# Kernel optimization log

Hardware: AMD Instinct MI355X
Metric: run time of the kernel (lower is better)

## Reference

```python
import jax, jax.numpy as jnp
import numpy as np

TK = 3          # number of temporal scales (wavedec level = TK-1)
SK = 3          # spatial rank count per scale (SK-1 rank-1 terms + residual)
INPUT_LEN = 256
N_NODES = 256
K = 32          # randomized-SVD sketch size
INV_SQRT2 = np.float32(1.0 / np.sqrt(2.0))


def haar_wavedec(x, levels):
    # x: (..., L) with L divisible by 2**levels; pywt haar, mode='zero', even L
    # returns [cD1, cD2, ..., cD_levels, cA_levels]  (== pywt.wavedec(...)[::-1])
    coeffs = []
    for _ in range(levels):
        L = x.shape[-1]
        pairs = x.reshape(x.shape[:-1] + (L // 2, 2))
        a, b = pairs[..., 0], pairs[..., 1]
        coeffs.append((a - b) * INV_SQRT2)  # detail cD
        x = (a + b) * INV_SQRT2             # approx cA
    coeffs.append(x)
    return coeffs


def setup_inputs() -> dict:
    key = jax.random.key(0)
    kx, kp = jax.random.split(key)
    x = jax.random.normal(kx, (4, INPUT_LEN, 64, N_NODES), dtype=jnp.float32)
    p = jax.random.normal(kp, (N_NODES, K), dtype=jnp.float32)
    return {"x": x, "p": p}


def reference(x, p):
    # x: (B, T, c, n) -> permute(0,2,3,1) -> (B, c, n, T)
    xw = jnp.transpose(x, (0, 2, 3, 1))
    coeffs = haar_wavedec(xw, TK - 1)  # TK tensors (B, c, n, L_i)
    res = []
    for xi in coeffs:
        if SK == 1:
            res.append(xi)
            continue
        xt = jnp.transpose(xi, (0, 3, 1, 2))          # (B, L, c, n)
        z = xt @ p                                     # (B, L, c, k)
        q, _ = jnp.linalg.qr(z)                        # reduced: (B, L, c, k)
        y = jnp.einsum('blck,blcn->blkn', q, xt)       # (B, L, k, n)
        u, s, vh = jnp.linalg.svd(y, full_matrices=False)  # u:(B,L,k,k) s:(B,L,k) vh:(B,L,k,n)
        u = q @ u                                      # (B, L, c, k)
        # rank-1 terms s_j * u_j v_j^T for j < SK-1, vectorized over j
        terms = jnp.einsum('blcj,blj,bljn->jblcn',
                           u[..., :SK - 1], s[..., :SK - 1], vh[..., :SK - 1, :])
        terms = jnp.transpose(terms, (0, 1, 3, 4, 2))  # (SK-1, B, c, n, L)
        resid = xi - terms.sum(axis=0)
        for j in range(SK - 1):
            res.append(terms[j])
        res.append(resid)
    # left-pad last dim to INPUT_LEN, then stack -> (TK*SK, B, c, n, INPUT_LEN)
    res = [jnp.pad(r, ((0, 0), (0, 0), (0, 0), (INPUT_LEN - r.shape[-1], 0))) for r in res]
    return jnp.stack(res)
```

## Files before the change

kernel.cpp:

```cpp
#include <hip/hip_runtime.h>

#define IS2f 0.70710678118654752440f

#define WS_Z   0ul
#define WS_G   2097152ul
#define WS_H   3145728ul
#define WS_SU  4194304ul
#define WS_VV  4325376ul
#define WS_B   4849664ul

#define WSYNC() asm volatile("" ::: "memory")

__device__ __forceinline__ float frcp(float v){ return __builtin_amdgcn_rcpf(v); }
__device__ __forceinline__ float frsq(float v){ return __builtin_amdgcn_rsqf(v); }
__device__ __forceinline__ float fsq (float v){ return __builtin_amdgcn_sqrtf(v); }
__device__ __forceinline__ float readlane_f(float v, int sl){
  return __uint_as_float(__builtin_amdgcn_readlane(__float_as_uint(v), sl));
}

__device__ __forceinline__ void decode_pid(int pid, int& ci, int& b, int& l, int& L){
  if (pid < 512)      { ci = 0; b = pid >> 7; l = pid & 127; L = 128; }
  else if (pid < 768) { int q = pid - 512; ci = 1; b = q >> 6; l = q & 63; L = 64; }
  else                { int q = pid - 768; ci = 2; b = q >> 6; l = q & 63; L = 64; }
}
__device__ __forceinline__ int su_base(int ci){ return ci==0 ? 0 : (ci==1 ? 65536 : 98304); }
__device__ __forceinline__ int vv_base(int ci){ return ci==0 ? 0 : (ci==1 ? 262144 : 393216); }
__device__ __forceinline__ int tpp(int r, int m){ return (m==0) ? r  : (r+m)%31; }
__device__ __forceinline__ int tqq(int r, int m){ return (m==0) ? 31 : (r+31-m)%31; }
__device__ __forceinline__ void jparam(float app, float aqq, float apq,
                                       float& cc, float& ss){
  float tau = (aqq - app) * frcp(2.f*apq);
  float tt  = ((tau>=0.f)?1.f:-1.f) * frcp(fabsf(tau) + fsq(fmaf(tau,tau,1.f)));
  float c   = frsq(fmaf(tt,tt,1.f));
  float s   = tt*c;
  bool ok = fabsf(apq) > 1e-28f;
  cc = ok ? c : 1.f;
  ss = ok ? s : 0.f;
}

#define PTS 260

__global__ __launch_bounds__(512) void k_fact(const float* __restrict__ x,
                                              const float* __restrict__ p,
                                              float* __restrict__ ws, int storeB){
  __shared__ __align__(16) float Ms[64*256];
  __shared__ __align__(16) float Zs[64*32];
  __shared__ __align__(16) float Pt[32*PTS];
  __shared__ __align__(16) float Bn[32*PTS];
  __shared__ float Gl[33*33];

  int pid = blockIdx.x, tid = threadIdx.x;
  int ci,b,l,L; decode_pid(pid,ci,b,l,L);

  {
    const float4* p4 = (const float4*)p;
    #pragma unroll
    for (int e=0;e<4;++e){
      int idx = tid + 512*e;
      int n = idx >> 3, k4 = idx & 7;
      float4 v = p4[idx];
      Pt[(4*k4+0)*PTS + n] = v.x;
      Pt[(4*k4+1)*PTS + n] = v.y;
      Pt[(4*k4+2)*PTS + n] = v.z;
      Pt[(4*k4+3)*PTS + n] = v.w;
    }
  }
  const float4* x4 = (const float4*)x;
  float4* Ms4 = (float4*)Ms;
  if (ci == 0){
    size_t base = ((size_t)(b*256 + 2*l) * 64) * 64;
    #pragma unroll
    for (int e=0;e<8;++e){
      int f = tid + 512*e;
      float4 A = x4[base + f];
      float4 Bv = x4[base + 4096 + f];
      float4 m;
      m.x=(A.x-Bv.x)*IS2f; m.y=(A.y-Bv.y)*IS2f; m.z=(A.z-Bv.z)*IS2f; m.w=(A.w-Bv.w)*IS2f;
      Ms4[f] = m;
    }
  } else {
    float sg = (ci==1) ? -0.5f : 0.5f;
    size_t base = ((size_t)(b*256 + 4*l) * 64) * 64;
    #pragma unroll
    for (int e=0;e<8;++e){
      int f = tid + 512*e;
      float4 A = x4[base + f];
      float4 B1 = x4[base + 4096 + f];
      float4 C1 = x4[base + 8192 + f];
      float4 D1 = x4[base + 12288 + f];
      float4 m;
      m.x=(A.x+B1.x)*0.5f + (C1.x+D1.x)*sg;
      m.y=(A.y+B1.y)*0.5f + (C1.y+D1.y)*sg;
      m.z=(A.z+B1.z)*0.5f + (C1.z+D1.z)*sg;
      m.w=(A.w+B1.w)*0.5f + (C1.w+D1.w)*sg;
      Ms4[f] = m;
    }
  }
  __syncthreads();

  {
    int k = tid & 31, c0 = tid >> 5;
    float acc[4] = {0,0,0,0};
    for (int n4=0;n4<64;++n4){
      float4 pv = *(const float4*)&Pt[k*PTS + 4*n4];
      #pragma unroll
      for (int i=0;i<4;++i){
        float4 m = Ms4[(c0*4+i)*64 + n4];
        acc[i] += m.x*pv.x + m.y*pv.y + m.z*pv.z + m.w*pv.w;
      }
    }
    #pragma unroll
    for (int i=0;i<4;++i){
      int c = c0*4 + i;
      Zs[c*32+k] = acc[i];
      ws[WS_Z + (size_t)pid*2048 + c*32 + k] = acc[i];
    }
  }
  __syncthreads();

  {
    int kk = tid & 31, j0 = tid >> 5;
    float ga[2] = {0,0};
    for (int c=0;c<64;++c){
      float zk = Zs[c*32+kk];
      #pragma unroll
      for (int e=0;e<2;++e) ga[e] += Zs[c*32 + j0 + 16*e] * zk;
    }
    #pragma unroll
    for (int e=0;e<2;++e)
      Gl[(j0+16*e)*33 + kk] = ga[e];
  }

  {
    int n4 = tid & 63, kg = tid >> 6;
    float4 facc[4];
    #pragma unroll
    for (int kq=0;kq<4;++kq){ facc[kq].x=0.f; facc[kq].y=0.f; facc[kq].z=0.f; facc[kq].w=0.f; }
    for (int c=0;c<64;++c){
      float4 mv = Ms4[c*64 + n4];
      float4 z1 = *(const float4*)&Zs[c*32 + kg*4];
      float zz[4] = {z1.x,z1.y,z1.z,z1.w};
      #pragma unroll
      for (int kq=0;kq<4;++kq){
        facc[kq].x += zz[kq]*mv.x; facc[kq].y += zz[kq]*mv.y;
        facc[kq].z += zz[kq]*mv.z; facc[kq].w += zz[kq]*mv.w;
      }
    }
    #pragma unroll
    for (int kq=0;kq<4;++kq){
      int krow = kg*4 + kq;
      *(float4*)&Bn[krow*PTS + 4*n4] = facc[kq];
      if (storeB)
        *(float4*)&ws[WS_B + (size_t)pid*8192 + (size_t)krow*256 + 4*n4] = facc[kq];
    }
  }
  __syncthreads();

  {
    int jlane = tid & 31, grp = tid >> 5;
    for (int k=0;k<32;++k){
      float gkk  = Gl[k*33+k];
      float ginv = frcp(gkk);
      float gkj  = Gl[k*33+jlane];
      float av[2], bv[2];
      #pragma unroll
      for (int e=0;e<2;++e){
        int i = k+1+grp+16*e; int ii = (i<32)? i : 31;
        av[e] = Gl[ii*33+jlane];
        bv[e] = Gl[k*33+ii];
      }
      WSYNC();
      #pragma unroll
      for (int e=0;e<2;++e){
        int i = k+1+grp+16*e;
        if (i < 32) Gl[i*33+jlane] = av[e] - bv[e]*gkj*ginv;
      }
      __syncthreads();
    }
    float sv[2];
    #pragma unroll
    for (int e=0;e<2;++e){
      int i = grp+16*e;
      sv[e] = Gl[i*33+jlane] * frsq(Gl[i*33+i]);
    }
    WSYNC();
    #pragma unroll
    for (int e=0;e<2;++e){
      int i = grp+16*e;
      Gl[i*33+jlane] = sv[e];
    }
  }
  __syncthreads();

  #pragma unroll
  for (int e=0;e<2;++e){
    int idx = tid + 512*e;
    ws[WS_G + (size_t)pid*1024 + idx] = Gl[(idx>>5)*33 + (idx&31)];
  }

  if (tid < 256){
    int n = tid;
    float c[32];
    #pragma unroll
    for (int i=0;i<32;++i){
      float cv = Bn[i*PTS + n];
      #pragma unroll
      for (int k=0;k<i;++k) cv -= Gl[k*33+i]*c[k];
      c[i] = cv * frcp(Gl[i*33+i]);
    }
    #pragma unroll
    for (int i=0;i<32;++i) Bn[i*PTS + n] = c[i];
  }
  __syncthreads();

  {
    int kk = tid & 31, j0 = tid >> 5;
    float h[2] = {0,0};
    for (int n4=0;n4<64;++n4){
      float4 bk = *(const float4*)&Bn[kk*PTS + 4*n4];
      #pragma unroll
      for (int e=0;e<2;++e){
        float4 bj = *(const float4*)&Bn[(j0+16*e)*PTS + 4*n4];
        h[e] += bj.x*bk.x + bj.y*bk.y + bj.z*bk.z + bj.w*bk.w;
      }
    }
    #pragma unroll
    for (int e=0;e<2;++e)
      ws[WS_H + (size_t)pid*1024 + (j0+16*e)*32 + kk] = h[e];
  }
}

#define NSWEEP 5

__global__ __launch_bounds__(128) void k_solve(const float* __restrict__ x,
                                               float* __restrict__ ws, int useB){
  __shared__ float Gs[32*33];
  __shared__ float Hb[2][32*33];
  __shared__ __align__(16) float Vb[2][32*36];
  __shared__ float cA2[2][16], sA2[2][16];
  __shared__ float ggs[2][32];
  __shared__ float uss[2][64];

  int pid = blockIdx.x, tid = threadIdx.x;
  int wave = tid >> 6;
  int lane = tid & 63;
  int jlane = tid & 31;
  int hlf  = (tid >> 5) & 1;
  int ci,b,l,L; decode_pid(pid,ci,b,l,L);

  #pragma unroll
  for (int e=0;e<8;++e){
    int idx = tid + 128*e; int i = idx>>5, j = idx&31;
    Gs[i*33+j]    = ws[WS_G + (size_t)pid*1024 + idx];
    Hb[0][i*33+j] = ws[WS_H + (size_t)pid*1024 + idx];
  }
  #pragma unroll
  for (int e=0;e<9;++e) Vb[0][tid + 128*e] = 0.f;
  __syncthreads();
  if (tid < 32) Vb[0][tid*36 + tid] = 1.f;
  __syncthreads();

  float dmx = (lane < 32) ? fabsf(Hb[0][jlane*33+jlane]) : 0.f;
  #pragma unroll
  for (int off=1; off<64; off<<=1) dmx = fmaxf(dmx, __shfl_xor(dmx, off));
  float thr = dmx * 3e-6f;

  int m2 = (lane >> 3) + 8*wave;
  int g  = lane & 7;
  int cur = 0;

  for (int sw=0; sw<NSWEEP; ++sw){
    for (int r=0; r<31; ++r){
      float* Hc = Hb[cur];
      float* Hn = Hb[cur^1];
      float4* Vc4 = (float4*)Vb[cur];
      float4* Vn4 = (float4*)Vb[cur^1];

      int m = lane & 15;
      int pm = tpp(r,m), qm = tqq(r,m);
      float apq = Hc[pm*33+qm];
      if (!__ballot(fabsf(apq) > thr)) continue;
      float app = Hc[pm*33+pm];
      float aqq = Hc[qm*33+qm];
      float cc, ssv; jparam(app, aqq, apq, cc, ssv);
      if (lane < 16){ cA2[wave][lane] = cc; sA2[wave][lane] = ssv; }
      WSYNC();

      int p2 = tpp(r,m2), q2 = tqq(r,m2);
      float c2 = cA2[wave][m2], s2 = sA2[wave][m2];

      float a_[2], b_[2], c_[2], d_[2], c1v[2], s1v[2];
      int p1v[2], q1v[2];
      #pragma unroll
      for (int e=0;e<2;++e){
        int m1 = g + 8*e;
        int p1 = tpp(r,m1), q1 = tqq(r,m1);
        p1v[e]=p1; q1v[e]=q1;
        c1v[e]=cA2[wave][m1]; s1v[e]=sA2[wave][m1];
        a_[e] = Hc[p1*33+p2]; b_[e] = Hc[p1*33+q2];
        c_[e] = Hc[q1*33+p2]; d_[e] = Hc[q1*33+q2];
      }
      float4 vp = Vc4[p2*9 + g];
      float4 vq = Vc4[q2*9 + g];

      #pragma unroll
      for (int e=0;e<2;++e){
        float c1 = c1v[e], s1 = s1v[e];
        float a1 = c1*a_[e] - s1*c_[e];
        float b1 = c1*b_[e] - s1*d_[e];
        float c1r= s1*a_[e] + c1*c_[e];
        float d1 = s1*b_[e] + c1*d_[e];
        Hn[p1v[e]*33+p2] = c2*a1 - s2*b1;
        Hn[p1v[e]*33+q2] = s2*a1 + c2*b1;
        Hn[q1v[e]*33+p2] = c2*c1r - s2*d1;
        Hn[q1v[e]*33+q2] = s2*c1r + c2*d1;
      }
      float4 np, nq;
      np.x = c2*vp.x - s2*vq.x;  nq.x = s2*vp.x + c2*vq.x;
      np.y = c2*vp.y - s2*vq.y;  nq.y = s2*vp.y + c2*vq.y;
      np.z = c2*vp.z - s2*vq.z;  nq.z = s2*vp.z + c2*vq.z;
      np.w = c2*vp.w - s2*vq.w;  nq.w = s2*vp.w + c2*vq.w;
      Vn4[p2*9 + g] = np;
      Vn4[q2*9 + g] = nq;
      __syncthreads();
      cur ^= 1;
    }
  }
  __syncthreads();
  if (wave == 1) return;

  float* Hs = Hb[cur];
  float* Vt = Vb[cur];

  float rdgr = frcp(Gs[jlane*33+jlane]);

  float dv = (lane < 32) ? Hs[jlane*33+jlane] : -3e38f;
  float m1r = dv;
  #pragma unroll
  for (int off=1; off<64; off<<=1) m1r = fmaxf(m1r, __shfl_xor(m1r, off));
  unsigned long long bm = __ballot(dv == m1r);
  int i0 = __ffsll((unsigned long long)bm) - 1;
  float dv2 = (lane == i0) ? -3e38f : dv;
  float m2r = dv2;
  #pragma unroll
  for (int off=1; off<64; off<<=1) m2r = fmaxf(m2r, __shfl_xor(m2r, off));
  unsigned long long bm2 = __ballot(dv2 == m2r);
  int i1 = __ffsll((unsigned long long)bm2) - 1;

  float lam = hlf ? m2r : m1r;
  int   ti  = hlf ? i1 : i0;
  float sj  = fsq(fmaxf(lam, 0.f)); sj = fmaxf(sj, 1e-12f);
  float s0 = readlane_f(sj, 0);
  float s1 = readlane_f(sj, 32);

  {
    float rr = Vt[ti*36 + jlane];
    float Greg[32];
    #pragma unroll
    for (int i=0;i<32;++i) Greg[i] = Gs[jlane*33+i];
    #pragma unroll
    for (int i=31;i>=0;--i){
      float ri = __shfl(rr,  hlf*32 + i);
      float di = __shfl(rdgr, i);
      float g  = ri * di;
      if (jlane == i) ggs[hlf][i] = g;
      if (jlane < i)  rr -= Greg[i]*g;
    }
  }
  WSYNC();

  {
    const float4* Z4 = (const float4*)(ws + WS_Z + (size_t)pid*2048);
    float u0 = 0.f, u1 = 0.f;
    #pragma unroll
    for (int k4=0;k4<8;++k4){
      float4 z = Z4[lane*8 + k4];
      u0 += z.x*ggs[0][k4*4+0] + z.y*ggs[0][k4*4+1] + z.z*ggs[0][k4*4+2] + z.w*ggs[0][k4*4+3];
      u1 += z.x*ggs[1][k4*4+0] + z.y*ggs[1][k4*4+1] + z.z*ggs[1][k4*4+2] + z.w*ggs[1][k4*4+3];
    }
    uss[0][lane] = u0; uss[1][lane] = u1;
    ws[WS_SU + su_base(ci) + ((size_t)(b*2+0)*64 + lane)*L + l] = s0*u0;
    ws[WS_SU + su_base(ci) + ((size_t)(b*2+1)*64 + lane)*L + l] = s1*u1;
  }
  WSYNC();

  float i0s = frcp(s0), i1s = frcp(s1);
  size_t vb0 = WS_VV + vv_base(ci) + ((size_t)(b*2+0)*L + l)*256 + lane*4;
  size_t vb1 = WS_VV + vv_base(ci) + ((size_t)(b*2+1)*L + l)*256 + lane*4;

  if (useB){
    const float4* B4 = (const float4*)(ws + WS_B + (size_t)pid*8192);
    float a0x=0,a0y=0,a0z=0,a0w=0, a1x=0,a1y=0,a1z=0,a1w=0;
    #pragma unroll 8
    for (int k=0;k<32;++k){
      float4 bv = B4[(size_t)k*64 + lane];
      float g0 = ggs[0][k], g1 = ggs[1][k];
      a0x += g0*bv.x; a0y += g0*bv.y; a0z += g0*bv.z; a0w += g0*bv.w;
      a1x += g1*bv.x; a1y += g1*bv.y; a1z += g1*bv.z; a1w += g1*bv.w;
    }
    float4 r0; r0.x=a0x*i0s; r0.y=a0y*i0s; r0.z=a0z*i0s; r0.w=a0w*i0s;
    float4 r1; r1.x=a1x*i1s; r1.y=a1y*i1s; r1.z=a1z*i1s; r1.w=a1w*i1s;
    *(float4*)(ws + vb0) = r0;
    *(float4*)(ws + vb1) = r1;
  } else {
    float a0x=0,a0y=0,a0z=0,a0w=0, a1x=0,a1y=0,a1z=0,a1w=0;
    const float4* x4 = (const float4*)x;
    if (ci == 0){
      size_t base = ((size_t)(b*256 + 2*l) * 64) * 64;
      #pragma unroll 2
      for (int c=0;c<64;++c){
        float4 A  = x4[base + c*64 + lane];
        float4 Bv = x4[base + 4096 + c*64 + lane];
        float mx=(A.x-Bv.x)*IS2f, my=(A.y-Bv.y)*IS2f, mz=(A.z-Bv.z)*IS2f, mw=(A.w-Bv.w)*IS2f;
        float uc0 = uss[0][c], uc1 = uss[1][c];
        a0x += uc0*mx; a0y += uc0*my; a0z += uc0*mz; a0w += uc0*mw;
        a1x += uc1*mx; a1y += uc1*my; a1z += uc1*mz; a1w += uc1*mw;
      }
    } else {
      float sg = (ci==1) ? -0.5f : 0.5f;
      size_t base = ((size_t)(b*256 + 4*l) * 64) * 64;
      #pragma unroll 2
      for (int c=0;c<64;++c){
        float4 A  = x4[base + c*64 + lane];
        float4 B1 = x4[base + 4096 + c*64 + lane];
        float4 C1 = x4[base + 8192 + c*64 + lane];
        float4 D1 = x4[base + 12288 + c*64 + lane];
        float mx=(A.x+B1.x)*0.5f + (C1.x+D1.x)*sg;
        float my=(A.y+B1.y)*0.5f + (C1.y+D1.y)*sg;
        float mz=(A.z+B1.z)*0.5f + (C1.z+D1.z)*sg;
        float mw=(A.w+B1.w)*0.5f + (C1.w+D1.w)*sg;
        float uc0 = uss[0][c], uc1 = uss[1][c];
        a0x += uc0*mx; a0y += uc0*my; a0z += uc0*mz; a0w += uc0*mw;
        a1x += uc1*mx; a1y += uc1*my; a1z += uc1*mz; a1w += uc1*mw;
      }
    }
    ws[vb0+0]=a0x*i0s; ws[vb0+1]=a0y*i0s; ws[vb0+2]=a0z*i0s; ws[vb0+3]=a0w*i0s;
    ws[vb1+0]=a1x*i1s; ws[vb1+1]=a1y*i1s; ws[vb1+2]=a1z*i1s; ws[vb1+3]=a1w*i1s;
  }
}

__global__ __launch_bounds__(256) void k_out(const float* __restrict__ x,
                                             const float* __restrict__ ws,
                                             float* __restrict__ out){
  __shared__ float d1[128*33];
  __shared__ float d2[64*33];
  __shared__ float a2s[64*33];
  __shared__ float Vs[2*128*33];
  __shared__ float Us[512];

  int nt = blockIdx.x, c = blockIdx.y, b = blockIdx.z;
  int n0 = nt * 32, tid = threadIdx.x;
  float* a1 = Vs;

  const float4* x4 = (const float4*)x;
  #pragma unroll
  for (int e=0;e<4;++e){
    int f = tid + 256*e; int l1 = f>>3, d4 = f&7;
    size_t r = ((size_t)(b*256 + 2*l1)*64 + c)*64 + (n0>>2) + d4;
    float4 A = x4[r], Bv = x4[r + 4096];
    int o = l1*33 + 4*d4;
    d1[o+0]=(A.x-Bv.x)*IS2f; d1[o+1]=(A.y-Bv.y)*IS2f; d1[o+2]=(A.z-Bv.z)*IS2f; d1[o+3]=(A.w-Bv.w)*IS2f;
    a1[o+0]=(A.x+Bv.x)*IS2f; a1[o+1]=(A.y+Bv.y)*IS2f; a1[o+2]=(A.z+Bv.z)*IS2f; a1[o+3]=(A.w+Bv.w)*IS2f;
  }
  __syncthreads();
  #pragma unroll
  for (int e=0;e<2;++e){
    int f = tid + 256*e; int l2 = f>>3, d4 = f&7;
    #pragma unroll
    for (int j=0;j<4;++j){
      int dn = 4*d4 + j;
      float aa = a1[(2*l2)*33 + dn], bb = a1[(2*l2+1)*33 + dn];
      d2[l2*33+dn]  = (aa-bb)*IS2f;
      a2s[l2*33+dn] = (aa+bb)*IS2f;
    }
  }
  #pragma unroll
  for (int e=0;e<2;++e){
    int idx = tid + 256*e;
    int j, l, L, so;
    if (idx < 256)      { j=idx>>7;        l=idx&127; L=128; so=0; }
    else if (idx < 384) { j=(idx-256)>>6;  l=idx&63;  L=64;  so=65536; }
    else                { j=(idx-384)>>6;  l=idx&63;  L=64;  so=98304; }
    Us[idx] = ws[WS_SU + so + ((size_t)(b*2+j)*64 + c)*L + l];
  }
  __syncthreads();

  for (int cc=0; cc<3; ++cc){
    int L   = (cc==0) ? 128 : 64;
    int pad = 256 - L;
    int sb  = cc*3;
    int uo  = (cc==0) ? 0 : (cc==1) ? 256 : 384;
    const float* cf = (cc==0) ? d1 : (cc==1) ? d2 : a2s;

    int iters = (2*L*32) >> 8;
    for (int e=0;e<iters;++e){
      int idx = tid + 256*e;
      int j = (idx >= L*32) ? 1 : 0;
      int rem = idx - j*L*32;
      int ll = rem >> 5, dn = rem & 31;
      Vs[j*4224 + ll*33 + dn] =
        ws[WS_VV + vv_base(cc) + ((size_t)(b*2+j)*L + ll)*256 + n0 + dn];
    }
    __syncthreads();

    int l = tid - pad;
    bool inr = (l >= 0);
    size_t obase = (size_t)sb*16777216 + (size_t)b*4194304 + (size_t)c*65536
                 + (size_t)n0*256 + tid;
    #pragma unroll 4
    for (int dn=0; dn<32; ++dn){
      float v0 = 0.f, v1 = 0.f, rv = 0.f;
      if (inr){
        float q0 = Us[uo + l]     * Vs[l*33 + dn];
        float q1 = Us[uo + L + l] * Vs[4224 + l*33 + dn];
        v0 = q0; v1 = q1;
        rv = cf[l*33 + dn] - q0 - q1;
      }
      out[obase + dn*256]            = v0;
      out[obase + dn*256 + 16777216] = v1;
      out[obase + dn*256 + 33554432] = rv;
    }
    __syncthreads();
  }
}

extern "C" void kernel_launch(void* const* d_in, const int* in_sizes, int n_in,
                              void* d_out, int out_size, void* d_ws, size_t ws_size,
                              hipStream_t stream) {
  const float* x = (const float*)d_in[0];
  const float* p = (const float*)d_in[1];
  float* out = (float*)d_out;
  float* ws  = (float*)d_ws;

  int useB = (ws_size >= (size_t)(WS_B + 1024ull*8192ull) * 4ull) ? 1 : 0;

  k_fact <<<1024, 512, 0, stream>>>(x, p, ws, useB);
  k_solve<<<1024, 128, 0, stream>>>(x, ws, useB);
  k_out  <<<dim3(8,64,4), 256, 0, stream>>>(x, ws, out);
}
```

Before: 426.4 us.

## Cut k_fact shared memory by dropping Pt/Bn and reusing Ms for the solved basis

Removes the transposed P and B staging buffers from shared memory in k_fact, so P is read directly from global memory and B is always written to the workspace. The triangular solve now reads B back from global, stores the solved C into the freed Ms buffer, and writes C back to the workspace. k_solve then forms V from C weighted by the eigenvector instead of from B weighted by the solved coefficients. The aim is to shrink LDS usage enough to fit more 512-thread blocks per CU, at the cost of extra global traffic and uncoalesced P loads.

```diff
diff --git a/kernel.cpp b/kernel.cpp
--- a/kernel.cpp
+++ b/kernel.cpp
@@ -40,31 +40,16 @@
 
 #define PTS 260
 
-__global__ __launch_bounds__(512) void k_fact(const float* __restrict__ x,
-                                              const float* __restrict__ p,
-                                              float* __restrict__ ws, int storeB){
+__global__ __launch_bounds__(512, 4) void k_fact(const float* __restrict__ x,
+                                                 const float* __restrict__ p,
+                                                 float* __restrict__ ws, int storeB){
   __shared__ __align__(16) float Ms[64*256];
   __shared__ __align__(16) float Zs[64*32];
-  __shared__ __align__(16) float Pt[32*PTS];
-  __shared__ __align__(16) float Bn[32*PTS];
   __shared__ float Gl[33*33];
 
   int pid = blockIdx.x, tid = threadIdx.x;
   int ci,b,l,L; decode_pid(pid,ci,b,l,L);
 
-  {
-    const float4* p4 = (const float4*)p;
-    #pragma unroll
-    for (int e=0;e<4;++e){
-      int idx = tid + 512*e;
-      int n = idx >> 3, k4 = idx & 7;
-      float4 v = p4[idx];
-      Pt[(4*k4+0)*PTS + n] = v.x;
-      Pt[(4*k4+1)*PTS + n] = v.y;
-      Pt[(4*k4+2)*PTS + n] = v.z;
-      Pt[(4*k4+3)*PTS + n] = v.w;
-    }
-  }
   const float4* x4 = (const float4*)x;
   float4* Ms4 = (float4*)Ms;
   if (ci == 0){
@@ -102,11 +87,14 @@
     int k = tid & 31, c0 = tid >> 5;
     float acc[4] = {0,0,0,0};
     for (int n4=0;n4<64;++n4){
-      float4 pv = *(const float4*)&Pt[k*PTS + 4*n4];
+      float p0 = p[(4*n4+0)*32 + k];
+      float p1 = p[(4*n4+1)*32 + k];
+      float p2 = p[(4*n4+2)*32 + k];
+      float p3 = p[(4*n4+3)*32 + k];
       #pragma unroll
       for (int i=0;i<4;++i){
         float4 m = Ms4[(c0*4+i)*64 + n4];
-        acc[i] += m.x*pv.x + m.y*pv.y + m.z*pv.z + m.w*pv.w;
+        acc[i] += m.x*p0 + m.y*p1 + m.z*p2 + m.w*p3;
       }
     }
     #pragma unroll
@@ -149,9 +137,7 @@
     #pragma unroll
     for (int kq=0;kq<4;++kq){
       int krow = kg*4 + kq;
-      *(float4*)&Bn[krow*PTS + 4*n4] = facc[kq];
-      if (storeB)
-        *(float4*)&ws[WS_B + (size_t)pid*8192 + (size_t)krow*256 + 4*n4] = facc[kq];
+      *(float4*)&ws[WS_B + (size_t)pid*8192 + (size_t)krow*256 + 4*n4] = facc[kq];
     }
   }
   __syncthreads();
@@ -198,18 +184,26 @@
     ws[WS_G + (size_t)pid*1024 + idx] = Gl[(idx>>5)*33 + (idx&31)];
   }
 
+  float* Cs = Ms;
   if (tid < 256){
     int n = tid;
+    float bcol[32];
+    #pragma unroll
+    for (int i=0;i<32;++i)
+      bcol[i] = ws[WS_B + (size_t)pid*8192 + (size_t)i*256 + n];
     float c[32];
     #pragma unroll
     for (int i=0;i<32;++i){
-      float cv = Bn[i*PTS + n];
+      float cv = bcol[i];
       #pragma unroll
       for (int k=0;k<i;++k) cv -= Gl[k*33+i]*c[k];
       c[i] = cv * frcp(Gl[i*33+i]);
     }
     #pragma unroll
-    for (int i=0;i<32;++i) Bn[i*PTS + n] = c[i];
+    for (int i=0;i<32;++i){
+      Cs[i*PTS + n] = c[i];
+      ws[WS_B + (size_t)pid*8192 + (size_t)i*256 + n] = c[i];
+    }
   }
   __syncthreads();
 
@@ -217,10 +211,10 @@
     int kk = tid & 31, j0 = tid >> 5;
     float h[2] = {0,0};
     for (int n4=0;n4<64;++n4){
-      float4 bk = *(const float4*)&Bn[kk*PTS + 4*n4];
+      float4 bk = *(const float4*)&Cs[kk*PTS + 4*n4];
       #pragma unroll
       for (int e=0;e<2;++e){
-        float4 bj = *(const float4*)&Bn[(j0+16*e)*PTS + 4*n4];
+        float4 bj = *(const float4*)&Cs[(j0+16*e)*PTS + 4*n4];
         h[e] += bj.x*bk.x + bj.y*bk.y + bj.z*bk.z + bj.w*bk.w;
       }
     }
@@ -239,6 +233,7 @@
   __shared__ __align__(16) float Vb[2][32*36];
   __shared__ float cA2[2][16], sA2[2][16];
   __shared__ float ggs[2][32];
+  __shared__ float wws[2][32];
   __shared__ float uss[2][64];
 
   int pid = blockIdx.x, tid = threadIdx.x;
@@ -355,6 +350,7 @@
 
   {
     float rr = Vt[ti*36 + jlane];
+    wws[hlf][jlane] = rr;
     float Greg[32];
     #pragma unroll
     for (int i=0;i<32;++i) Greg[i] = Gs[jlane*33+i];
@@ -389,14 +385,14 @@
   size_t vb1 = WS_VV + vv_base(ci) + ((size_t)(b*2+1)*L + l)*256 + lane*4;
 
   if (useB){
-    const float4* B4 = (const float4*)(ws + WS_B + (size_t)pid*8192);
+    const float4* C4 = (const float4*)(ws + WS_B + (size_t)pid*8192);
     float a0x=0,a0y=0,a0z=0,a0w=0, a1x=0,a1y=0,a1z=0,a1w=0;
     #pragma unroll 8
     for (int k=0;k<32;++k){
-      float4 bv = B4[(size_t)k*64 + lane];
-      float g0 = ggs[0][k], g1 = ggs[1][k];
-      a0x += g0*bv.x; a0y += g0*bv.y; a0z += g0*bv.z; a0w += g0*bv.w;
-      a1x += g1*bv.x; a1y += g1*bv.y; a1z += g1*bv.z; a1w += g1*bv.w;
+      float4 cv = C4[(size_t)k*64 + lane];
+      float w0 = wws[0][k], w1 = wws[1][k];
+      a0x += w0*cv.x; a0y += w0*cv.y; a0z += w0*cv.z; a0w += w0*cv.w;
+      a1x += w1*cv.x; a1y += w1*cv.y; a1z += w1*cv.z; a1w += w1*cv.w;
     }
     float4 r0; r0.x=a0x*i0s; r0.y=a0y*i0s; r0.z=a0z*i0s; r0.w=a0w*i0s;
     float4 r1; r1.x=a1x*i1s; r1.y=a1y*i1s; r1.z=a1z*i1s; r1.w=a1w*i1s;
```

Result: faster. 403.1 us (median of 2 runs) (-5.5%).
